# Kernel optimization log

Hardware: AMD Instinct MI355X
Metric: run time of the kernel (lower is better)

Reference implementation:

```python
import jax, jax.numpy as jnp
import numpy as np

HIDDEN = 2048
NUM_HEADS = 16
HEAD_DIM = HIDDEN // NUM_HEADS  # 128
ROPE_BASE = 10000.0


def setup_inputs() -> dict:
    key = jax.random.key(0)
    ks = jax.random.split(key, 5)
    B, T, C = 2, 2048, HIDDEN
    scale = 1.0 / np.sqrt(C)
    x = jax.random.normal(ks[0], (B, T, C), dtype=jnp.float32)
    Wq = jax.random.normal(ks[1], (C, C), dtype=jnp.float32) * scale
    Wk = jax.random.normal(ks[2], (C, C), dtype=jnp.float32) * scale
    Wv = jax.random.normal(ks[3], (C, C), dtype=jnp.float32) * scale
    Wo = jax.random.normal(ks[4], (C, C), dtype=jnp.float32) * scale
    return {"x": x, "Wq": Wq, "Wk": Wk, "Wv": Wv, "Wo": Wo}


def _rope_cos_sin(T, dtype):
    # inv_freq: [D/2]; emb: [T, D] = cat(freqs, freqs)
    inv_freq = 1.0 / (ROPE_BASE ** (jnp.arange(0, HEAD_DIM, 2, dtype=jnp.float32) / HEAD_DIM))
    t = jnp.arange(T, dtype=jnp.float32)
    freqs = t[:, None] * inv_freq[None, :]          # [T, D/2]
    emb = jnp.concatenate([freqs, freqs], axis=-1)  # [T, D]
    # broadcast shape [1, T, 1, D] to match q/k [B, T, H, D]
    return jnp.cos(emb)[None, :, None, :].astype(dtype), jnp.sin(emb)[None, :, None, :].astype(dtype)


def _rotate_half(u):
    u1, u2 = jnp.split(u, 2, axis=-1)
    return jnp.concatenate([-u2, u1], axis=-1)


def reference(x, Wq, Wk, Wv, Wo):
    B, T, C = x.shape
    H, D = NUM_HEADS, HEAD_DIM
    # QKV projections (torch Linear: x @ W.T). Weights here stored as [C, C] so use x @ W.
    q = (x @ Wq).reshape(B, T, H, D)
    k = (x @ Wk).reshape(B, T, H, D)
    v = (x @ Wv).reshape(B, T, H, D)
    cos, sin = _rope_cos_sin(T, x.dtype)
    q = q * cos + _rotate_half(q) * sin
    k = k * cos + _rotate_half(k) * sin
    # causal SDPA: scores [B, H, T, T]
    scale = 1.0 / jnp.sqrt(jnp.asarray(D, dtype=x.dtype))
    scores = jnp.einsum('bqhd,bkhd->bhqk', q, k) * scale
    causal = jnp.tril(jnp.ones((T, T), dtype=bool))
    scores = jnp.where(causal[None, None, :, :], scores, jnp.asarray(-jnp.inf, dtype=scores.dtype))
    attn = jax.nn.softmax(scores, axis=-1)
    out = jnp.einsum('bhqk,bkhd->bqhd', attn, v).reshape(B, T, C)
    return out @ Wo
```

## Files before the change

kernel.cpp:

```cpp
#include <hip/hip_runtime.h>
#include <hip/hip_bf16.h>

#define C_DIM 2048
#define NHEAD 16
#define HD 128
#define BB 2
#define TT 2048
#define MM (BB * TT)
#define NQT 32
#define N3 (3 * C_DIM)

typedef short short4v __attribute__((ext_vector_type(4)));
typedef short short8v __attribute__((ext_vector_type(8)));
typedef __bf16 bf16x4 __attribute__((ext_vector_type(4)));
typedef __bf16 bf16x8 __attribute__((ext_vector_type(8)));
typedef float f32x4 __attribute__((ext_vector_type(4)));

#define AS1 __attribute__((address_space(1)))
#define AS3 __attribute__((address_space(3)))

#define VMCNT(n) asm volatile("s_waitcnt vmcnt(" #n ")" ::: "memory")

__device__ __forceinline__ void load_lds16(const void* g, void* l) {
  __builtin_amdgcn_global_load_lds((const AS1 void*)g, (AS3 void*)l, 16, 0, 0);
}

__device__ __forceinline__ short f2bf(float f) {
  union { float f; unsigned u; } v; v.f = f;
  unsigned u = v.u;
  u += 0x7FFFu + ((u >> 16) & 1u);
  return (short)(u >> 16);
}
__device__ __forceinline__ float bf2f(short s) {
  union { unsigned u; float f; } v;
  v.u = ((unsigned)(unsigned short)s) << 16;
  return v.f;
}

__device__ __forceinline__ float exp2_fast(float x) {
  float r;
  asm("v_exp_f32 %0, %1" : "=v"(r) : "v"(x));
  return r;
}

__global__ __launch_bounds__(256) void cvt_x(const float* __restrict__ in,
                                             short* __restrict__ out, int n4) {
  int i = blockIdx.x * 256 + threadIdx.x;
  int stride = gridDim.x * 256;
  for (int idx = i; idx < n4; idx += stride) {
    float4 f = ((const float4*)in)[idx];
    short4v o;
    o[0] = f2bf(f.x); o[1] = f2bf(f.y); o[2] = f2bf(f.z); o[3] = f2bf(f.w);
    ((short4v*)out)[idx] = o;
  }
}

__global__ __launch_bounds__(256) void cvt_w_all(const float* __restrict__ Wq,
                                                 const float* __restrict__ Wk,
                                                 const float* __restrict__ Wv,
                                                 const float* __restrict__ Wo,
                                                 short* __restrict__ Wt) {
  __shared__ float tile[32][33];
  int z = blockIdx.z;
  const float* W = z == 0 ? Wq : z == 1 ? Wk : z == 2 ? Wv : Wo;
  short* dst = Wt + (size_t)z * C_DIM * C_DIM;
  int bx = blockIdx.x;
  int by = blockIdx.y;
  int lx = threadIdx.x & 31;
  int ly = threadIdx.x >> 5;
#pragma unroll
  for (int j = 0; j < 4; ++j) {
    int r = by * 32 + ly + j * 8;
    tile[ly + j * 8][lx] = W[(size_t)r * C_DIM + bx * 32 + lx];
  }
  __syncthreads();
#pragma unroll
  for (int j = 0; j < 4; ++j) {
    int n = bx * 32 + ly + j * 8;
    dst[(size_t)n * C_DIM + by * 32 + lx] = f2bf(tile[lx][ly + j * 8]);
  }
}

__global__ __launch_bounds__(256) void rope_tab(float2* __restrict__ tab) {
  int idx = blockIdx.x * 256 + threadIdx.x;
  int t = idx >> 6, d = idx & 63;
  float inv = expf(-9.210340371976184f * (float)d * (1.0f / 64.0f));
  float a = (float)t * inv;
  tab[idx] = make_float2(cosf(a), sinf(a));
}

template <bool F32OUT>
__global__ __launch_bounds__(256, 2) void gemm8p(const short* __restrict__ A,
                                                 const short* __restrict__ Bt,
                                                 void* __restrict__ Cout,
                                                 int M, int N, int K, int NBN) {
  __shared__ short sA[2][128 * 64];
  __shared__ short sB[2][128 * 64];
  const int tid = threadIdx.x;
  const int lane = tid & 63;
  const int w = tid >> 6;
  const int wm = w >> 1, wn = w & 1;
  const int r = lane & 15, g = lane >> 4;

  const int wg = blockIdx.x;
  const int mb = wg / NBN, nb = wg % NBN;
  const int m0 = mb * 128, n0 = nb * 128;

  f32x4 acc[4][4] = {};

  auto stage = [&](int buf, int kt) {
#pragma unroll
    for (int j = 0; j < 4; ++j) {
      int p = j * 256 + tid;
      int row = p >> 3;
      int c16 = (p & 7) ^ (row & 7);
      load_lds16(A + (size_t)(m0 + row) * K + kt * 64 + c16 * 8,
                 &sA[buf][(j * 256 + w * 64) * 8]);
    }
#pragma unroll
    for (int j = 0; j < 4; ++j) {
      int p = j * 256 + tid;
      int row = p >> 3;
      int c16 = (p & 7) ^ (row & 7);
      load_lds16(Bt + (size_t)(n0 + row) * K + kt * 64 + c16 * 8,
                 &sB[buf][(j * 256 + w * 64) * 8]);
    }
  };

  auto compute = [&](int buf) {
#pragma unroll
    for (int kk = 0; kk < 2; ++kk) {
      bf16x8 af[4], bv[4];
#pragma unroll
      for (int m = 0; m < 4; ++m) {
        int row = wm * 64 + m * 16 + r;
        af[m] = *(const bf16x8*)((const char*)&sA[buf][0] + row * 128 +
                                 (((kk * 4 + g) ^ (row & 7)) << 4));
      }
#pragma unroll
      for (int n = 0; n < 4; ++n) {
        int row = wn * 64 + n * 16 + r;
        bv[n] = *(const bf16x8*)((const char*)&sB[buf][0] + row * 128 +
                                 (((kk * 4 + g) ^ (row & 7)) << 4));
      }
      __builtin_amdgcn_s_setprio(1);
#pragma unroll
      for (int m = 0; m < 4; ++m)
#pragma unroll
        for (int n = 0; n < 4; ++n)
          acc[m][n] = __builtin_amdgcn_mfma_f32_16x16x32_bf16(af[m], bv[n], acc[m][n], 0, 0, 0);
      __builtin_amdgcn_s_setprio(0);
    }
  };

  const int NT = K >> 6;
  stage(0, 0);
  stage(1, 1);
  VMCNT(8);
  __builtin_amdgcn_s_barrier();

  for (int t = 0; t < NT; ++t) {
    const int cur = t & 1;
    compute(cur);
    if (t + 1 < NT) {
      asm volatile("" ::: "memory");
      __builtin_amdgcn_s_barrier();
      if (t + 2 < NT) {
        stage(cur, t + 2);
        VMCNT(8);
      } else {
        VMCNT(0);
      }
      asm volatile("" ::: "memory");
      __builtin_amdgcn_s_barrier();
    }
  }

#pragma unroll
  for (int m = 0; m < 4; ++m)
#pragma unroll
    for (int n = 0; n < 4; ++n)
#pragma unroll
      for (int q = 0; q < 4; ++q) {
        int row = m0 + wm * 64 + m * 16 + g * 4 + q;
        int col = n0 + wn * 64 + n * 16 + r;
        size_t off = (size_t)row * N + col;
        if constexpr (F32OUT) ((float*)Cout)[off] = acc[m][n][q];
        else ((short*)Cout)[off] = f2bf(acc[m][n][q]);
      }
}

__global__ __launch_bounds__(256) void rope_qk(const short* __restrict__ qkv,
                                               const float2* __restrict__ tab,
                                               short* __restrict__ Qr,
                                               short* __restrict__ Kr) {
  const short* src = qkv + (blockIdx.y ? C_DIM : 0);
  short* dst = blockIdx.y ? Kr : Qr;
  const float qs = blockIdx.y ? 1.0f : 0.12751744f;
  int rid = blockIdx.x * 4 + (threadIdx.x >> 6);
  int lane = threadIdx.x & 63;
  int t = rid & (TT - 1);
  int bh = rid >> 11;
  int b = bh >> 4, h = bh & 15;
  const short* in = src + ((size_t)(b * TT + t)) * N3 + h * HD;

  int v = *(const int*)(in + 2 * lane);
  int pv = __shfl_xor(v, 32, 64);
  float f0 = bf2f((short)(v & 0xFFFF)),  f1 = bf2f((short)(v >> 16));
  float p0 = bf2f((short)(pv & 0xFFFF)), p1 = bf2f((short)(pv >> 16));
  float4 cst = *(const float4*)(tab + (size_t)t * 64 + ((2 * lane) & 63));
  float s = (lane < 32) ? -1.0f : 1.0f;
  float o0 = (f0 * cst.x + s * p0 * cst.y) * qs;
  float o1 = (f1 * cst.z + s * p1 * cst.w) * qs;
  unsigned out2 = ((unsigned)(unsigned short)f2bf(o0)) |
                  (((unsigned)(unsigned short)f2bf(o1)) << 16);
  *(unsigned*)(dst + (size_t)rid * HD + 2 * lane) = out2;
}

__global__ __launch_bounds__(256) void v_tr(const short* __restrict__ qkv,
                                            short* __restrict__ Vt) {
  __shared__ short tl[64][132];
  int bh = blockIdx.y, b = bh >> 4, h = bh & 15;
  int t0 = blockIdx.x * 64;
  int tid = threadIdx.x;
  const short* vsrc = qkv + 2 * C_DIM;
#pragma unroll
  for (int i = 0; i < 4; ++i) {
    int c = i * 256 + tid;
    int row = c >> 4, cc = c & 15;
    short8v v = *(const short8v*)(vsrc + ((size_t)(b * TT + t0 + row)) * N3 + h * HD + cc * 8);
#pragma unroll
    for (int j = 0; j < 8; ++j) tl[row][cc * 8 + j] = v[j];
  }
  __syncthreads();
  int d = tid >> 1, half = tid & 1;
#pragma unroll
  for (int u = 0; u < 4; ++u) {
    short8v ov;
#pragma unroll
    for (int j = 0; j < 8; ++j) ov[j] = tl[half * 32 + u * 8 + j][d];
    *(short8v*)(Vt + ((size_t)bh * HD + d) * TT + t0 + half * 32 + u * 8) = ov;
  }
}

__global__ __launch_bounds__(256, 3) void attn_one(const short* __restrict__ Qr,
                                                   const short* __restrict__ Kr,
                                                   const short* __restrict__ Vt,
                                                   short* __restrict__ AO) {
  const int bx = blockIdx.x;
  const int j = bx >> 5, bh = bx & 31;
  const int qt = (j & 1) ? (j >> 1) : (NQT - 1 - (j >> 1));
  const int b = bh >> 4, h = bh & 15;
  const int tid = threadIdx.x;
  const int lane = tid & 63;
  const int w = tid >> 6;
  const int r = lane & 15, g = lane >> 4;

  __shared__ short sK[64 * 128];
  __shared__ short sV[128 * 64];
  __shared__ short sP[4][16 * 64];

  bf16x8 qf[4];
  {
    const short* qbp = Qr + ((size_t)bh * TT + qt * 64 + w * 16 + r) * HD + g * 8;
#pragma unroll
    for (int s = 0; s < 4; ++s) qf[s] = *(const bf16x8*)(qbp + s * 32);
  }

  f32x4 o[8] = {};
  float m = -1e30f, l = 0.f;

  short8v kreg[4], vreg[4];
  auto stage_load = [&](int kt) {
#pragma unroll
    for (int i = 0; i < 4; ++i) {
      int c = i * 256 + tid;
      kreg[i] = *(const short8v*)(Kr + ((size_t)bh * TT + kt * 64 + (c >> 4)) * HD + (c & 15) * 8);
    }
#pragma unroll
    for (int i = 0; i < 4; ++i) {
      int c = i * 256 + tid;
      vreg[i] = *(const short8v*)(Vt + ((size_t)bh * HD + (c >> 3)) * TT + kt * 64 + (c & 7) * 8);
    }
  };
  auto stage_write = [&]() {
#pragma unroll
    for (int i = 0; i < 4; ++i) {
      int c = i * 256 + tid;
      int row = c >> 4, cc = c & 15;
      int addr = (row * 256 + cc * 16) ^ ((row & 7) << 4);
      *(short8v*)((char*)sK + addr) = kreg[i];
    }
#pragma unroll
    for (int i = 0; i < 4; ++i) {
      int c = i * 256 + tid;
      int row = c >> 3, cc = c & 7;
      int addr = (row * 128 + cc * 16) ^ ((row & 7) << 4);
      *(short8v*)((char*)sV + addr) = vreg[i];
    }
  };

  char* pw = (char*)&sP[w][0];

  stage_load(0);
  stage_write();
  __syncthreads();

  for (int kt = 0; kt <= qt; ++kt) {
    f32x4 sacc[4] = {};
    __builtin_amdgcn_s_setprio(1);
#pragma unroll
    for (int nf = 0; nf < 4; ++nf) {
#pragma unroll
      for (int ss = 0; ss < 4; ++ss) {
        int krow = nf * 16 + r;
        int addr = (krow * 256 + (ss * 32 + g * 8) * 2) ^ ((krow & 7) << 4);
        bf16x8 kf = *(const bf16x8*)((char*)sK + addr);
        sacc[nf] = __builtin_amdgcn_mfma_f32_16x16x32_bf16(kf, qf[ss], sacc[nf], 0, 0, 0);
      }
    }
    __builtin_amdgcn_s_setprio(0);

    if (kt < qt) stage_load(kt + 1);

    if (kt == qt) {
#pragma unroll
      for (int nf = 0; nf < 4; ++nf)
#pragma unroll
        for (int q = 0; q < 4; ++q)
          if (nf * 16 + g * 4 + q > w * 16 + r) sacc[nf][q] = -1e30f;
    }

    float p01 = fmaxf(fmaxf(sacc[0][0], sacc[0][1]), fmaxf(sacc[0][2], sacc[0][3]));
    float p23 = fmaxf(fmaxf(sacc[1][0], sacc[1][1]), fmaxf(sacc[1][2], sacc[1][3]));
    float p45 = fmaxf(fmaxf(sacc[2][0], sacc[2][1]), fmaxf(sacc[2][2], sacc[2][3]));
    float p67 = fmaxf(fmaxf(sacc[3][0], sacc[3][1]), fmaxf(sacc[3][2], sacc[3][3]));
    float pmax = fmaxf(fmaxf(p01, p23), fmaxf(p45, p67));
    pmax = fmaxf(pmax, __shfl_xor(pmax, 16, 64));
    pmax = fmaxf(pmax, __shfl_xor(pmax, 32, 64));

    if (!__all(pmax - m <= 8.0f)) {
      float mnew = fmaxf(m, pmax);
      float alpha = exp2_fast(m - mnew);
      m = mnew;
      l *= alpha;
#pragma unroll
      for (int q = 0; q < 4; ++q) {
        float aq = __shfl(alpha, (g * 4 + q) | (lane & 48), 64);
#pragma unroll
        for (int nf2 = 0; nf2 < 8; ++nf2) o[nf2][q] *= aq;
      }
    }

    float s16 = 0.f;
#pragma unroll
    for (int nf = 0; nf < 4; ++nf) {
      f32x4 pe;
#pragma unroll
      for (int q = 0; q < 4; ++q) pe[q] = exp2_fast(sacc[nf][q] - m);
      s16 += (pe[0] + pe[1]) + (pe[2] + pe[3]);
      int addr = (r * 128 + nf * 32 + g * 8) ^ ((r & 7) << 4);
      *(bf16x4*)(pw + addr) = __builtin_convertvector(pe, bf16x4);
    }
    float rs = s16;
    rs += __shfl_xor(rs, 16, 64);
    rs += __shfl_xor(rs, 32, 64);
    l += rs;

    __builtin_amdgcn_s_setprio(1);
#pragma unroll
    for (int s2 = 0; s2 < 2; ++s2) {
      int paddr = (r * 128 + s2 * 64 + g * 16) ^ ((r & 7) << 4);
      bf16x8 pa = *(const bf16x8*)(pw + paddr);
#pragma unroll
      for (int nf2 = 0; nf2 < 8; ++nf2) {
        int drow = nf2 * 16 + r;
        int addr = (drow * 128 + (s2 * 32 + g * 8) * 2) ^ ((drow & 7) << 4);
        bf16x8 vb = *(const bf16x8*)((char*)sV + addr);
        o[nf2] = __builtin_amdgcn_mfma_f32_16x16x32_bf16(pa, vb, o[nf2], 0, 0, 0);
      }
    }
    __builtin_amdgcn_s_setprio(0);

    __syncthreads();
    if (kt < qt) {
      stage_write();
      __syncthreads();
    }
  }

  float linv = 1.0f / l;
  float lrow[4];
#pragma unroll
  for (int q = 0; q < 4; ++q)
    lrow[q] = __shfl(linv, (g * 4 + q) | (lane & 48), 64);
  short* ow = sK + w * 16 * 128;
#pragma unroll
  for (int nf2 = 0; nf2 < 8; ++nf2)
#pragma unroll
    for (int q = 0; q < 4; ++q)
      ow[(g * 4 + q) * 128 + nf2 * 16 + r] = f2bf(o[nf2][q] * lrow[q]);
  __syncthreads();

#pragma unroll
  for (int ch = 0; ch < 4; ++ch) {
    int c = ch * 256 + tid;
    int orow = c >> 4;
    int ocol = (c & 15) * 8;
    int t = qt * 64 + orow;
    *(short8v*)(AO + ((size_t)b * TT + t) * C_DIM + h * HD + ocol) =
        *(const short8v*)(sK + orow * 128 + ocol);
  }
}

extern "C" void kernel_launch(void* const* d_in, const int* in_sizes, int n_in,
                              void* d_out, int out_size, void* d_ws, size_t ws_size,
                              hipStream_t stream) {
  const float* x  = (const float*)d_in[0];
  const float* Wq = (const float*)d_in[1];
  const float* Wk = (const float*)d_in[2];
  const float* Wv = (const float*)d_in[3];
  const float* Wo = (const float*)d_in[4];

  char* ws = (char*)d_ws;
  size_t off = 0;
  auto take = [&](size_t bytes) {
    char* p = ws + off;
    off += (bytes + 255) & ~(size_t)255;
    return p;
  };
  const size_t xe = (size_t)MM * C_DIM;
  const size_t we = (size_t)C_DIM * C_DIM;
  short* xb   = (short*)take(xe * 2);
  short* wqkv = (short*)take(4 * we * 2);
  short* wot  = wqkv + 3 * we;
  short* qkv  = (short*)take(3 * xe * 2);
  short* Qr   = (short*)take(xe * 2);
  short* Kr   = (short*)take(xe * 2);
  short* Vtr  = (short*)take(xe * 2);
  float2* tab = (float2*)take((size_t)TT * 64 * sizeof(float2));
  short* AO   = qkv;

  cvt_x<<<2048, 256, 0, stream>>>(x, xb, (int)(xe / 4));
  cvt_w_all<<<dim3(64, 64, 4), 256, 0, stream>>>(Wq, Wk, Wv, Wo, wqkv);
  rope_tab<<<(TT * 64) / 256, 256, 0, stream>>>(tab);

  gemm8p<false><<<1536, 256, 0, stream>>>(xb, wqkv, qkv, MM, N3, C_DIM, N3 / 128);

  rope_qk<<<dim3(16384, 2), 256, 0, stream>>>(qkv, tab, Qr, Kr);
  v_tr<<<dim3(32, 32), 256, 0, stream>>>(qkv, Vtr);

  attn_one<<<1024, 256, 0, stream>>>(Qr, Kr, Vtr, AO);

  gemm8p<true><<<512, 256, 0, stream>>>(AO, wot, d_out, MM, C_DIM, C_DIM, C_DIM / 128);
}
```

Baseline: 290.1 us.

## Rewrite GEMM as 256x128 tile, 8-wave, triple-buffered pipeline

The GEMM kernel now uses 512-thread blocks computing 256x128 tiles, with three LDS stages instead of two. Global-to-LDS prefetch for tile T+2 is interleaved between the two half-steps of compute, so loads overlap MFMA work. B tiles are reused across more M rows, which reduces global traffic per FLOP. In exchange, LDS use grows to about 144KB per block, which lowers occupancy, and the output-projection GEMM launches only 256 blocks, which may underfill the GPU.

```diff
diff --git a/kernel.cpp b/kernel.cpp
--- a/kernel.cpp
+++ b/kernel.cpp
@@ -90,12 +90,12 @@
 }
 
 template <bool F32OUT>
-__global__ __launch_bounds__(256, 2) void gemm8p(const short* __restrict__ A,
+__global__ __launch_bounds__(512, 2) void gemm3p(const short* __restrict__ A,
                                                  const short* __restrict__ Bt,
                                                  void* __restrict__ Cout,
                                                  int M, int N, int K, int NBN) {
-  __shared__ short sA[2][128 * 64];
-  __shared__ short sB[2][128 * 64];
+  __shared__ short sA[3][256 * 64];
+  __shared__ short sB[3][128 * 64];
   const int tid = threadIdx.x;
   const int lane = tid & 63;
   const int w = tid >> 6;
@@ -104,89 +104,101 @@
 
   const int wg = blockIdx.x;
   const int mb = wg / NBN, nb = wg % NBN;
-  const int m0 = mb * 128, n0 = nb * 128;
+  const int m0 = mb * 256, n0 = nb * 128;
 
   f32x4 acc[4][4] = {};
 
-  auto stage = [&](int buf, int kt) {
-#pragma unroll
-    for (int j = 0; j < 4; ++j) {
-      int p = j * 256 + tid;
+  auto stageA = [&](int buf, int kt) {
+#pragma unroll
+    for (int j2 = 0; j2 < 4; ++j2) {
+      int p = j2 * 512 + tid;
       int row = p >> 3;
-      int c16 = (p & 7) ^ (row & 7);
-      load_lds16(A + (size_t)(m0 + row) * K + kt * 64 + c16 * 8,
-                 &sA[buf][(j * 256 + w * 64) * 8]);
-    }
-#pragma unroll
-    for (int j = 0; j < 4; ++j) {
-      int p = j * 256 + tid;
+      int srcg = (p & 7) ^ (row & 7);
+      load_lds16(A + (size_t)(m0 + row) * K + kt * 64 + srcg * 8,
+                 &sA[buf][(j2 * 512 + w * 64) * 8]);
+    }
+  };
+  auto stageB = [&](int buf, int kt) {
+#pragma unroll
+    for (int j2 = 0; j2 < 2; ++j2) {
+      int p = j2 * 512 + tid;
       int row = p >> 3;
-      int c16 = (p & 7) ^ (row & 7);
-      load_lds16(Bt + (size_t)(n0 + row) * K + kt * 64 + c16 * 8,
-                 &sB[buf][(j * 256 + w * 64) * 8]);
+      int srcg = (p & 7) ^ (row & 7);
+      load_lds16(Bt + (size_t)(n0 + row) * K + kt * 64 + srcg * 8,
+                 &sB[buf][(j2 * 512 + w * 64) * 8]);
     }
   };
 
-  auto compute = [&](int buf) {
-#pragma unroll
-    for (int kk = 0; kk < 2; ++kk) {
-      bf16x8 af[4], bv[4];
-#pragma unroll
-      for (int m = 0; m < 4; ++m) {
-        int row = wm * 64 + m * 16 + r;
-        af[m] = *(const bf16x8*)((const char*)&sA[buf][0] + row * 128 +
-                                 (((kk * 4 + g) ^ (row & 7)) << 4));
-      }
-#pragma unroll
-      for (int n = 0; n < 4; ++n) {
-        int row = wn * 64 + n * 16 + r;
-        bv[n] = *(const bf16x8*)((const char*)&sB[buf][0] + row * 128 +
-                                 (((kk * 4 + g) ^ (row & 7)) << 4));
-      }
+  const int NT = K >> 6;
+
+  stageA(0, 0); stageB(0, 0);
+  stageA(1, 1); stageB(1, 1);
+  VMCNT(6);
+  __builtin_amdgcn_s_barrier();
+
+  int bT = 0, bS = 2;
+  for (int T = 0; T < NT; ++T) {
+    const char* Ab = (const char*)&sA[bT][0];
+    const char* Bb = (const char*)&sB[bT][0];
+#pragma unroll
+    for (int qn = 0; qn < 2; ++qn) {
+      bf16x8 af[4][2], bv[2][2];
+#pragma unroll
+      for (int fi = 0; fi < 4; ++fi) {
+        int row = wm * 64 + fi * 16 + r;
+#pragma unroll
+        for (int kk = 0; kk < 2; ++kk)
+          af[fi][kk] = *(const bf16x8*)(Ab + row * 128 +
+                                        (((kk * 4 + g) ^ (row & 7)) << 4));
+      }
+#pragma unroll
+      for (int fj = 0; fj < 2; ++fj) {
+        int row = wn * 64 + qn * 32 + fj * 16 + r;
+#pragma unroll
+        for (int kk = 0; kk < 2; ++kk)
+          bv[fj][kk] = *(const bf16x8*)(Bb + row * 128 +
+                                        (((kk * 4 + g) ^ (row & 7)) << 4));
+      }
+
+      if (T + 2 < NT) {
+        if (qn == 0) stageA(bS, T + 2);
+        else         stageB(bS, T + 2);
+      }
+
+      __builtin_amdgcn_s_barrier();
+
       __builtin_amdgcn_s_setprio(1);
 #pragma unroll
-      for (int m = 0; m < 4; ++m)
-#pragma unroll
-        for (int n = 0; n < 4; ++n)
-          acc[m][n] = __builtin_amdgcn_mfma_f32_16x16x32_bf16(af[m], bv[n], acc[m][n], 0, 0, 0);
+      for (int fi = 0; fi < 4; ++fi)
+#pragma unroll
+        for (int fj = 0; fj < 2; ++fj)
+#pragma unroll
+          for (int kk = 0; kk < 2; ++kk)
+            acc[fi][qn * 2 + fj] = __builtin_amdgcn_mfma_f32_16x16x32_bf16(
+                af[fi][kk], bv[fj][kk], acc[fi][qn * 2 + fj], 0, 0, 0);
       __builtin_amdgcn_s_setprio(0);
-    }
-  };
-
-  const int NT = K >> 6;
-  stage(0, 0);
-  stage(1, 1);
-  VMCNT(8);
-  __builtin_amdgcn_s_barrier();
-
-  for (int t = 0; t < NT; ++t) {
-    const int cur = t & 1;
-    compute(cur);
-    if (t + 1 < NT) {
-      asm volatile("" ::: "memory");
+
+      if (qn == 1) {
+        if (T == NT - 2) { VMCNT(0); }
+        else if (T < NT - 2) { VMCNT(6); }
+      }
       __builtin_amdgcn_s_barrier();
-      if (t + 2 < NT) {
-        stage(cur, t + 2);
-        VMCNT(8);
-      } else {
-        VMCNT(0);
-      }
-      asm volatile("" ::: "memory");
-      __builtin_amdgcn_s_barrier();
-    }
-  }
-
-#pragma unroll
-  for (int m = 0; m < 4; ++m)
-#pragma unroll
-    for (int n = 0; n < 4; ++n)
+    }
+    bT = (bT == 2) ? 0 : bT + 1;
+    bS = (bS == 2) ? 0 : bS + 1;
+  }
+
+#pragma unroll
+  for (int fi = 0; fi < 4; ++fi)
+#pragma unroll
+    for (int nj = 0; nj < 4; ++nj)
 #pragma unroll
       for (int q = 0; q < 4; ++q) {
-        int row = m0 + wm * 64 + m * 16 + g * 4 + q;
-        int col = n0 + wn * 64 + n * 16 + r;
+        int row = m0 + wm * 64 + fi * 16 + g * 4 + q;
+        int col = n0 + wn * 64 + nj * 16 + r;
         size_t off = (size_t)row * N + col;
-        if constexpr (F32OUT) ((float*)Cout)[off] = acc[m][n][q];
-        else ((short*)Cout)[off] = f2bf(acc[m][n][q]);
+        if constexpr (F32OUT) ((float*)Cout)[off] = acc[fi][nj][q];
+        else ((short*)Cout)[off] = f2bf(acc[fi][nj][q]);
       }
 }
 
@@ -445,12 +457,12 @@
   cvt_w_all<<<dim3(64, 64, 4), 256, 0, stream>>>(Wq, Wk, Wv, Wo, wqkv);
   rope_tab<<<(TT * 64) / 256, 256, 0, stream>>>(tab);
 
-  gemm8p<false><<<1536, 256, 0, stream>>>(xb, wqkv, qkv, MM, N3, C_DIM, N3 / 128);
+  gemm3p<false><<<768, 512, 0, stream>>>(xb, wqkv, qkv, MM, N3, C_DIM, N3 / 128);
 
   rope_qk<<<dim3(16384, 2), 256, 0, stream>>>(qkv, tab, Qr, Kr);
   v_tr<<<dim3(32, 32), 256, 0, stream>>>(qkv, Vtr);
 
   attn_one<<<1024, 256, 0, stream>>>(Qr, Kr, Vtr, AO);
 
-  gemm8p<true><<<512, 256, 0, stream>>>(AO, wot, d_out, MM, C_DIM, C_DIM, C_DIM / 128);
-}
+  gemm3p<true><<<256, 512, 0, stream>>>(AO, wot, d_out, MM, C_DIM, C_DIM, C_DIM / 128);
+}
```

New measurement: 293.4 us. Within noise of the previous version (+1.1%).
